# Performance work log

Measured on AMD Instinct MI355X. Metric: run time of the kernel, lower is better.

## Reference

```python
import jax, jax.numpy as jnp
import numpy as np

B, T, D = 4, 2048, 1024
H = 16
HD = D // H


def setup_inputs() -> dict:
    key = jax.random.key(0)
    ks = jax.random.split(key, 9)
    s = 1.0 / np.sqrt(D)
    return {
        "x": jax.random.normal(ks[0], (B, T, D), dtype=jnp.float32),
        "Wk": jax.random.normal(ks[1], (D, D), dtype=jnp.float32) * s,
        "bk": jnp.zeros((D,), dtype=jnp.float32),
        "Wq": jax.random.normal(ks[2], (D, D), dtype=jnp.float32) * s,
        "bq": jnp.zeros((D,), dtype=jnp.float32),
        "Wv": jax.random.normal(ks[3], (D, D), dtype=jnp.float32) * s,
        "bv": jnp.zeros((D,), dtype=jnp.float32),
        "Wp": jax.random.normal(ks[4], (D, D), dtype=jnp.float32) * s,
        "bp": jnp.zeros((D,), dtype=jnp.float32),
    }


def reference(x, Wk, bk, Wq, bq, Wv, bv, Wp, bp):
    Bv, Tv, Dv = x.shape
    # project and split heads: [B, H, T, HD]
    def heads(w, b):
        return (x @ w + b).reshape(Bv, Tv, H, HD).transpose(0, 2, 1, 3)
    k = heads(Wk, bk)
    q = heads(Wq, bq)
    v = heads(Wv, bv)
    scale = 1.0 / np.sqrt(HD)
    att = jnp.einsum('bhqd,bhkd->bhqk', q, k) * scale  # [B,H,T,T]
    causal = jnp.tril(jnp.ones((Tv, Tv), dtype=bool))
    att = jnp.where(causal[None, None, :, :], att, -jnp.inf)
    att = jax.nn.softmax(att, axis=-1)
    y = jnp.einsum('bhqk,bhkd->bhqd', att, v)  # [B,H,T,HD]
    y = y.transpose(0, 2, 1, 3).reshape(Bv, Tv, Dv)
    return y @ Wp + bp
```

## Files before the change

kernel.cpp:

```cpp
#include <hip/hip_runtime.h>
#include <stdint.h>

#define Bb 4
#define Tt 2048
#define Dd 1024
#define Hh 16
#define HDd 64
#define Mm 8192

typedef __attribute__((ext_vector_type(8))) short bf16x8;
typedef __attribute__((ext_vector_type(4))) float f32x4;
typedef __attribute__((ext_vector_type(16))) float f32x16;

#define MFMA(a, b, c) __builtin_amdgcn_mfma_f32_16x16x32_bf16(a, b, c, 0, 0, 0)
#define MFMA32(a, b, c) __builtin_amdgcn_mfma_f32_32x32x16_bf16(a, b, c, 0, 0, 0)

#define LOG2E 1.44269504088896340736f
#if __has_builtin(__builtin_amdgcn_exp2f)
#define EXP2(x) __builtin_amdgcn_exp2f(x)
#else
#define EXP2(x) __expf((x) * 0.69314718055994530942f)
#endif

union vfu { uint2 u2[2]; bf16x8 v; };
union apu { uint32_t u[4]; bf16x8 v; };

__device__ __forceinline__ unsigned short f2b(float f) {
  union { float f; uint32_t u; } v; v.f = f;
  return (unsigned short)((v.u + 0x7FFFu + ((v.u >> 16) & 1u)) >> 16);
}

__device__ __forceinline__ uint32_t pk2(float a, float b) {
  union { __bf16 h[2]; uint32_t u; } x;
  x.h[0] = (__bf16)a; x.h[1] = (__bf16)b;
  return x.u;
}

__device__ __forceinline__ void gload_lds16(const void* g, void* l) {
  __builtin_amdgcn_global_load_lds(
      (const __attribute__((address_space(1))) void*)g,
      (__attribute__((address_space(3))) void*)l, 16, 0, 0);
}

__global__ __launch_bounds__(256) void k_convert_x(const float* __restrict__ x,
                                                   unsigned short* __restrict__ xb) {
  int i = (blockIdx.x * 256 + threadIdx.x) * 8;
  float4 a = *(const float4*)(x + i);
  float4 b = *(const float4*)(x + i + 4);
  uint4 o;
  o.x = f2b(a.x) | ((uint32_t)f2b(a.y) << 16);
  o.y = f2b(a.z) | ((uint32_t)f2b(a.w) << 16);
  o.z = f2b(b.x) | ((uint32_t)f2b(b.y) << 16);
  o.w = f2b(b.z) | ((uint32_t)f2b(b.w) << 16);
  *(uint4*)(xb + i) = o;
}

__global__ __launch_bounds__(256) void k_transpose_w(
    const float* __restrict__ Wk, const float* __restrict__ Wq,
    const float* __restrict__ Wv, const float* __restrict__ Wp,
    unsigned short* __restrict__ WkT, unsigned short* __restrict__ WqT,
    unsigned short* __restrict__ WvT, unsigned short* __restrict__ WpT) {
  const float* W; unsigned short* O;
  int wsel = blockIdx.y;
  W = wsel == 0 ? Wk : wsel == 1 ? Wq : wsel == 2 ? Wv : Wp;
  O = wsel == 0 ? WkT : wsel == 1 ? WqT : wsel == 2 ? WvT : WpT;
  __shared__ unsigned short tile[32][36];
  int kb = (blockIdx.x >> 5) << 5;
  int nb = (blockIdx.x & 31) << 5;
  int t = threadIdx.x;
  int r = t >> 3, c4 = (t & 7) << 2;
  float4 v = *(const float4*)(W + (size_t)(kb + r) * Dd + nb + c4);
  tile[r][c4 + 0] = f2b(v.x); tile[r][c4 + 1] = f2b(v.y);
  tile[r][c4 + 2] = f2b(v.z); tile[r][c4 + 3] = f2b(v.w);
  __syncthreads();
  uint2 o;
  o.x = tile[c4 + 0][r] | ((uint32_t)tile[c4 + 1][r] << 16);
  o.y = tile[c4 + 2][r] | ((uint32_t)tile[c4 + 3][r] << 16);
  *(uint2*)(O + (size_t)(nb + r) * Dd + kb + c4) = o;
}

__global__ __launch_bounds__(256, 2) void k_gemm3(
    const unsigned short* __restrict__ A,
    const unsigned short* __restrict__ BtQ, const unsigned short* __restrict__ BtK,
    const unsigned short* __restrict__ BtV,
    const float* __restrict__ bq, const float* __restrict__ bk,
    const float* __restrict__ bv,
    unsigned short* __restrict__ Qb, unsigned short* __restrict__ Kb,
    unsigned short* __restrict__ VTb) {
  __shared__ __align__(16) unsigned short Al[128 * 32];
  __shared__ __align__(16) unsigned short Bl[3][128 * 32];
  int tid = threadIdx.x;
  int lane = tid & 63, wid = tid >> 6;
  int wr = wid >> 1, wc = wid & 1;
  int lq = lane & 15, lh = lane >> 4;
  int mb = blockIdx.x * 128;
  int nb = blockIdx.y << 7;

  int srow = (wid << 5) + (lane >> 2);
  int scol = (lane & 3) << 3;
  const unsigned short* Ag = A + (size_t)(mb + srow) * Dd + scol;
  const unsigned short* Bg0 = BtQ + (size_t)(nb + srow) * Dd + scol;
  const unsigned short* Bg1 = BtK + (size_t)(nb + srow) * Dd + scol;
  const unsigned short* Bg2 = BtV + (size_t)(nb + srow) * Dd + scol;
  unsigned short* Alw = Al + (wid << 10);
  unsigned short* Blw0 = &Bl[0][0] + (wid << 10);
  unsigned short* Blw1 = &Bl[1][0] + (wid << 10);
  unsigned short* Blw2 = &Bl[2][0] + (wid << 10);

  f32x4 zero = {0.f, 0.f, 0.f, 0.f};
  f32x4 acc[3][4][4];
#pragma unroll
  for (int s = 0; s < 3; s++)
#pragma unroll
    for (int m = 0; m < 4; m++)
#pragma unroll
      for (int n = 0; n < 4; n++) acc[s][m][n] = zero;

  for (int kb = 0; kb < Dd; kb += 32) {
    __syncthreads();
    gload_lds16(Ag + kb, Alw);
    gload_lds16(Ag + kb + 16 * Dd, Alw + 16 * 32);
    gload_lds16(Bg0 + kb, Blw0);
    gload_lds16(Bg0 + kb + 16 * Dd, Blw0 + 16 * 32);
    gload_lds16(Bg1 + kb, Blw1);
    gload_lds16(Bg1 + kb + 16 * Dd, Blw1 + 16 * 32);
    gload_lds16(Bg2 + kb, Blw2);
    gload_lds16(Bg2 + kb + 16 * Dd, Blw2 + 16 * 32);
    __syncthreads();
    bf16x8 af[4];
#pragma unroll
    for (int m = 0; m < 4; m++)
      af[m] = *(const bf16x8*)(Al + (((wr << 6) + (m << 4) + lq) << 5) + (lh << 3));
#pragma unroll
    for (int s = 0; s < 3; s++) {
      bf16x8 bf[4];
#pragma unroll
      for (int n = 0; n < 4; n++)
        bf[n] = *(const bf16x8*)(&Bl[s][0] +
                                 (((wc << 6) + (n << 4) + lq) << 5) + (lh << 3));
      __builtin_amdgcn_s_setprio(1);
#pragma unroll
      for (int m = 0; m < 4; m++)
#pragma unroll
        for (int n = 0; n < 4; n++) acc[s][m][n] = MFMA(af[m], bf[n], acc[s][m][n]);
      __builtin_amdgcn_s_setprio(0);
    }
  }

  int b_idx = mb >> 11;
#pragma unroll
  for (int s = 0; s < 3; s++) {
#pragma unroll
    for (int n = 0; n < 4; n++) {
      int col = nb + (wc << 6) + (n << 4) + lq;
      float bbias = (s == 0) ? bq[col] : (s == 1) ? bk[col] : bv[col];
      int hh = col >> 6, hd = col & 63;
#pragma unroll
      for (int m = 0; m < 4; m++) {
        int row0 = mb + (wr << 6) + (m << 4) + (lh << 2);
        int t0 = row0 & 2047;
        if (s == 2) {
          float v0 = acc[s][m][n][0] + bbias, v1 = acc[s][m][n][1] + bbias;
          float v2 = acc[s][m][n][2] + bbias, v3 = acc[s][m][n][3] + bbias;
          uint2 pv;
          pv.x = f2b(v0) | ((uint32_t)f2b(v1) << 16);
          pv.y = f2b(v2) | ((uint32_t)f2b(v3) << 16);
          int t0s = t0 ^ ((hd & 7) << 3);
          *(uint2*)(VTb + ((size_t)(b_idx * 16 + hh) * 64 + hd) * Tt + t0s) = pv;
        } else {
          unsigned short* O = (s == 0) ? Qb : Kb;
          float sc = (s == 0) ? (0.125f * LOG2E) : 1.0f;
#pragma unroll
          for (int r = 0; r < 4; r++) {
            float v = (acc[s][m][n][r] + bbias) * sc;
            int trow = t0 + r;
            int hds = (s == 0) ? hd : (hd ^ ((trow & 7) << 3));
            O[((size_t)(b_idx * 16 + hh) * Tt + trow) * 64 + hds] = f2b(v);
          }
        }
      }
    }
  }
}

__global__ __launch_bounds__(256) void k_gemm(
    const unsigned short* __restrict__ A,
    const unsigned short* __restrict__ Bt0,
    const float* __restrict__ bias0,
    float* __restrict__ Pout) {
  __shared__ __align__(16) unsigned short Al[128 * 32];
  __shared__ __align__(16) unsigned short Bl[128 * 32];
  int tid = threadIdx.x;
  int lane = tid & 63, wid = tid >> 6;
  int wr = wid >> 1, wc = wid & 1;
  int lq = lane & 15, lh = lane >> 4;
  int mb = blockIdx.x * 128;
  int nb = blockIdx.y << 7;
  const unsigned short* Bt = Bt0; const float* bias = bias0;

  int srow = (wid << 5) + (lane >> 2);
  int scol = (lane & 3) << 3;
  const unsigned short* Ag = A + (size_t)(mb + srow) * Dd + scol;
  const unsigned short* Bg = Bt + (size_t)(nb + srow) * Dd + scol;
  unsigned short* Alw = Al + (wid << 10);
  unsigned short* Blw = Bl + (wid << 10);

  f32x4 zero = {0.f, 0.f, 0.f, 0.f};
  f32x4 acc[4][4];
#pragma unroll
  for (int m = 0; m < 4; m++)
#pragma unroll
    for (int n = 0; n < 4; n++) acc[m][n] = zero;

  for (int kb = 0; kb < Dd; kb += 32) {
    __syncthreads();
    gload_lds16(Ag + kb, Alw);
    gload_lds16(Ag + kb + 16 * Dd, Alw + 16 * 32);
    gload_lds16(Bg + kb, Blw);
    gload_lds16(Bg + kb + 16 * Dd, Blw + 16 * 32);
    __syncthreads();
    bf16x8 af[4], bf[4];
#pragma unroll
    for (int m = 0; m < 4; m++)
      af[m] = *(const bf16x8*)(Al + (((wr << 6) + (m << 4) + lq) << 5) + (lh << 3));
#pragma unroll
    for (int n = 0; n < 4; n++)
      bf[n] = *(const bf16x8*)(Bl + (((wc << 6) + (n << 4) + lq) << 5) + (lh << 3));
#pragma unroll
    for (int m = 0; m < 4; m++)
#pragma unroll
      for (int n = 0; n < 4; n++) acc[m][n] = MFMA(af[m], bf[n], acc[m][n]);
  }

#pragma unroll
  for (int n = 0; n < 4; n++) {
    int col = nb + (wc << 6) + (n << 4) + lq;
    float bb = bias[col];
#pragma unroll
    for (int m = 0; m < 4; m++) {
      int row0 = mb + (wr << 6) + (m << 4) + (lh << 2);
#pragma unroll
      for (int r = 0; r < 4; r++)
        Pout[(size_t)(row0 + r) * Dd + col] = acc[m][n][r] + bb;
    }
  }
}

__global__ __launch_bounds__(256, 2) void k_attn(
    const unsigned short* __restrict__ Qb, const unsigned short* __restrict__ Kb,
    const unsigned short* __restrict__ VTb, unsigned short* __restrict__ yb) {
  __shared__ __align__(16) unsigned short KL[2][8192];
  __shared__ __align__(16) unsigned short VL[2][8192];
  int b = blockIdx.x;
  int qt = (b < 256) ? (7 - (b >> 6)) : ((b - 256) >> 6);
  int rr6 = b & 63;
  int bh = ((rr6 & 7) << 3) | (rr6 >> 3);
  int tid = threadIdx.x, lane = tid & 63, w = tid >> 6;
  int l31 = lane & 31, hi = lane >> 5;
  const unsigned short* __restrict__ Qh = Qb + (size_t)bh * Tt * 64;
  const unsigned short* __restrict__ Kh = Kb + (size_t)bh * Tt * 64;
  const unsigned short* __restrict__ Vh = VTb + (size_t)bh * 64 * Tt;
  int qgA = (qt << 8) + (w << 6);
  int qgB = qgA + 32;

  bf16x8 qfA[4], qfB[4];
#pragma unroll
  for (int c = 0; c < 4; c++) {
    qfA[c] = *(const bf16x8*)(Qh + (size_t)(qgA + l31) * 64 + (c << 4) + (hi << 3));
    qfB[c] = *(const bf16x8*)(Qh + (size_t)(qgB + l31) * 64 + (c << 4) + (hi << 3));
  }

  f32x16 accA0, accA1, accB0, accB1;
#pragma unroll
  for (int i = 0; i < 16; i++) { accA0[i] = 0.f; accA1[i] = 0.f; accB0[i] = 0.f; accB1[i] = 0.f; }
  float lsumA = 0.f, lsumB = 0.f;

  int jmaxb = (qt << 1) + 1;
  int srowK = lane >> 3, scolK = (lane & 7) << 3;
  int rowbK = w << 5;
  int srowV = lane >> 4, scolV = (lane & 15) << 3;
  int rowbV = w << 4;
  int swz = l31 & 7;

#define STAGE(kvt_, bi_) do {                                                        \
    int kv_ = (kvt_) << 7;                                                           \
    gload_lds16(Kh + (size_t)(kv_ + rowbK + srowK) * 64 + scolK,                     \
                &KL[bi_][rowbK << 6]);                                               \
    gload_lds16(Kh + (size_t)(kv_ + rowbK + 8 + srowK) * 64 + scolK,                 \
                &KL[bi_][(rowbK + 8) << 6]);                                         \
    gload_lds16(Kh + (size_t)(kv_ + rowbK + 16 + srowK) * 64 + scolK,                \
                &KL[bi_][(rowbK + 16) << 6]);                                        \
    gload_lds16(Kh + (size_t)(kv_ + rowbK + 24 + srowK) * 64 + scolK,                \
                &KL[bi_][(rowbK + 24) << 6]);                                        \
    gload_lds16(Vh + (size_t)(rowbV + srowV) * Tt + kv_ + scolV,                     \
                &VL[bi_][rowbV << 7]);                                               \
    gload_lds16(Vh + (size_t)(rowbV + 4 + srowV) * Tt + kv_ + scolV,                 \
                &VL[bi_][(rowbV + 4) << 7]);                                         \
    gload_lds16(Vh + (size_t)(rowbV + 8 + srowV) * Tt + kv_ + scolV,                 \
                &VL[bi_][(rowbV + 8) << 7]);                                         \
    gload_lds16(Vh + (size_t)(rowbV + 12 + srowV) * Tt + kv_ + scolV,                \
                &VL[bi_][(rowbV + 12) << 7]);                                        \
  } while (0)

  STAGE(0, 0);
  __syncthreads();

  int cur = 0;
  for (int jt = 0; jt <= jmaxb; ++jt) {
    if (jt < jmaxb) STAGE(jt + 1, cur ^ 1);
    int base_kv = jt << 7;
    if (qgB >= base_kv) {
      const unsigned short* KB = &KL[cur][0];
      const unsigned short* VB = &VL[cur][0];
#pragma unroll
      for (int n2 = 0; n2 < 4; n2++) {
        int rel_base = qgA - base_kv - (n2 << 5);
        if (rel_base >= -32) {
          bf16x8 kf[4];
          int krowb = ((n2 << 5) + l31) << 6;
#pragma unroll
          for (int c = 0; c < 4; c++)
            kf[c] = *(const bf16x8*)(KB + krowb + ((((c << 1) + hi) ^ swz) << 3));
          f32x16 sA, sB;
#pragma unroll
          for (int i = 0; i < 16; i++) { sA[i] = 0.f; sB[i] = 0.f; }
          __builtin_amdgcn_s_setprio(1);
#pragma unroll
          for (int c = 0; c < 4; c++) {
            sA = MFMA32(kf[c], qfA[c], sA);
            sB = MFMA32(kf[c], qfB[c], sB);
          }
          __builtin_amdgcn_s_setprio(0);
          float pA[16], pB[16];
          if (rel_base <= 0) {
            int relA = rel_base + l31, relB = relA + 32;
#pragma unroll
            for (int r = 0; r < 16; r++) {
              int krow = (r & 3) + ((r >> 2) << 3) + (hi << 2);
              pA[r] = EXP2(krow > relA ? -1e30f : sA[r]);
              pB[r] = EXP2(krow > relB ? -1e30f : sB[r]);
            }
          } else {
#pragma unroll
            for (int r = 0; r < 16; r++) { pA[r] = EXP2(sA[r]); pB[r] = EXP2(sB[r]); }
          }
          lsumA += (((pA[0] + pA[1]) + (pA[2] + pA[3])) + ((pA[4] + pA[5]) + (pA[6] + pA[7])))
                 + (((pA[8] + pA[9]) + (pA[10] + pA[11])) + ((pA[12] + pA[13]) + (pA[14] + pA[15])));
          lsumB += (((pB[0] + pB[1]) + (pB[2] + pB[3])) + ((pB[4] + pB[5]) + (pB[6] + pB[7])))
                 + (((pB[8] + pB[9]) + (pB[10] + pB[11])) + ((pB[12] + pB[13]) + (pB[14] + pB[15])));
          vfu vf[2][2];
#pragma unroll
          for (int n2v = 0; n2v < 2; n2v++) {
            int vrowb = ((n2v << 5) + l31) << 7;
#pragma unroll
            for (int cc = 0; cc < 2; cc++) {
              int blk0 = (n2 << 2) + (cc << 1);
              vf[n2v][cc].u2[0] =
                  *(const uint2*)(VB + vrowb + ((blk0 ^ swz) << 3) + (hi << 2));
              vf[n2v][cc].u2[1] =
                  *(const uint2*)(VB + vrowb + (((blk0 + 1) ^ swz) << 3) + (hi << 2));
            }
          }
          apu a0, a1, b0, b1;
#pragma unroll
          for (int g = 0; g < 4; g++) {
            a0.u[g] = pk2(pA[2 * g], pA[2 * g + 1]);
            a1.u[g] = pk2(pA[8 + 2 * g], pA[8 + 2 * g + 1]);
            b0.u[g] = pk2(pB[2 * g], pB[2 * g + 1]);
            b1.u[g] = pk2(pB[8 + 2 * g], pB[8 + 2 * g + 1]);
          }
          __builtin_amdgcn_s_setprio(1);
          accA0 = MFMA32(a0.v, vf[0][0].v, accA0);
          accA1 = MFMA32(a0.v, vf[1][0].v, accA1);
          accB0 = MFMA32(b0.v, vf[0][0].v, accB0);
          accB1 = MFMA32(b0.v, vf[1][0].v, accB1);
          accA0 = MFMA32(a1.v, vf[0][1].v, accA0);
          accA1 = MFMA32(a1.v, vf[1][1].v, accA1);
          accB0 = MFMA32(b1.v, vf[0][1].v, accB0);
          accB1 = MFMA32(b1.v, vf[1][1].v, accB1);
          __builtin_amdgcn_s_setprio(0);
        }
      }
    }
    __syncthreads();
    cur ^= 1;
  }
#undef STAGE

  lsumA += __shfl_xor(lsumA, 32);
  lsumB += __shfl_xor(lsumB, 32);
  float invA = 1.0f / lsumA;
  float invB = 1.0f / lsumB;
  int bb = bh >> 4, hh = bh & 15;
#pragma unroll
  for (int r = 0; r < 16; r++) {
    int qr = (r & 3) + ((r >> 2) << 3) + (hi << 2);
    float invqA = __shfl(invA, qr);
    float invqB = __shfl(invB, qr);
    size_t baseA = ((size_t)(bb * Tt + qgA + qr)) * Dd + (hh << 6) + l31;
    size_t baseB = ((size_t)(bb * Tt + qgB + qr)) * Dd + (hh << 6) + l31;
    yb[baseA] = f2b(accA0[r] * invqA);
    yb[baseA + 32] = f2b(accA1[r] * invqA);
    yb[baseB] = f2b(accB0[r] * invqB);
    yb[baseB + 32] = f2b(accB1[r] * invqB);
  }
}

extern "C" void kernel_launch(void* const* d_in, const int* in_sizes, int n_in,
                              void* d_out, int out_size, void* d_ws, size_t ws_size,
                              hipStream_t stream) {
  const float* x = (const float*)d_in[0];
  const float* Wk = (const float*)d_in[1];
  const float* bk = (const float*)d_in[2];
  const float* Wq = (const float*)d_in[3];
  const float* bq = (const float*)d_in[4];
  const float* Wv = (const float*)d_in[5];
  const float* bv = (const float*)d_in[6];
  const float* Wp = (const float*)d_in[7];
  const float* bp = (const float*)d_in[8];
  float* out = (float*)d_out;

  char* ws = (char*)d_ws;
  unsigned short* xb  = (unsigned short*)(ws);
  unsigned short* WkT = (unsigned short*)(ws + (16ull << 20));
  unsigned short* WqT = (unsigned short*)(ws + (18ull << 20));
  unsigned short* WvT = (unsigned short*)(ws + (20ull << 20));
  unsigned short* WpT = (unsigned short*)(ws + (22ull << 20));
  unsigned short* Qb  = (unsigned short*)(ws + (24ull << 20));
  unsigned short* Kb  = (unsigned short*)(ws + (40ull << 20));
  unsigned short* VTb = (unsigned short*)(ws + (56ull << 20));
  unsigned short* yb  = (unsigned short*)(ws + (72ull << 20));

  k_convert_x<<<4096, 256, 0, stream>>>(x, xb);
  k_transpose_w<<<dim3(1024, 4), 256, 0, stream>>>(Wk, Wq, Wv, Wp, WkT, WqT, WvT, WpT);
  k_gemm3<<<dim3(64, 8), 256, 0, stream>>>(xb, WqT, WkT, WvT, bq, bk, bv,
                                           Qb, Kb, VTb);
  k_attn<<<512, 256, 0, stream>>>(Qb, Kb, VTb, yb);
  k_gemm<<<dim3(64, 8), 256, 0, stream>>>(yb, WpT, bp, out);
}
```

Baseline: 159.8 us.

## Widen output GEMM tile, compute softmax sums via MFMA, skip masked-out tiles

The output projection GEMM now gives each block 256 columns held as two B tiles that share one A tile, with half as many blocks in y, so A-tile reuse doubles. The attention kernel computes the softmax row sums with an extra MFMA against a ones vector instead of scalar adds and shuffles. It also skips the A-half QK and PV MFMAs when that sub-tile lies entirely above the causal diagonal. This cuts VALU reductions and wasted MFMA work, at the cost of extra MFMAs and accumulator registers, and the GEMM now has fewer blocks.

After: 171.8 us. 1.08x slower.

```diff
diff --git a/kernel.cpp b/kernel.cpp
--- a/kernel.cpp
+++ b/kernel.cpp
@@ -183,65 +183,80 @@
   }
 }
 
-__global__ __launch_bounds__(256) void k_gemm(
+__global__ __launch_bounds__(256, 2) void k_gemm(
     const unsigned short* __restrict__ A,
     const unsigned short* __restrict__ Bt0,
     const float* __restrict__ bias0,
     float* __restrict__ Pout) {
   __shared__ __align__(16) unsigned short Al[128 * 32];
-  __shared__ __align__(16) unsigned short Bl[128 * 32];
+  __shared__ __align__(16) unsigned short Bl[2][128 * 32];
   int tid = threadIdx.x;
   int lane = tid & 63, wid = tid >> 6;
   int wr = wid >> 1, wc = wid & 1;
   int lq = lane & 15, lh = lane >> 4;
   int mb = blockIdx.x * 128;
-  int nb = blockIdx.y << 7;
-  const unsigned short* Bt = Bt0; const float* bias = bias0;
+  int nb = blockIdx.y << 8;
 
   int srow = (wid << 5) + (lane >> 2);
   int scol = (lane & 3) << 3;
   const unsigned short* Ag = A + (size_t)(mb + srow) * Dd + scol;
-  const unsigned short* Bg = Bt + (size_t)(nb + srow) * Dd + scol;
+  const unsigned short* Bg0 = Bt0 + (size_t)(nb + srow) * Dd + scol;
+  const unsigned short* Bg1 = Bt0 + (size_t)(nb + 128 + srow) * Dd + scol;
   unsigned short* Alw = Al + (wid << 10);
-  unsigned short* Blw = Bl + (wid << 10);
+  unsigned short* Blw0 = &Bl[0][0] + (wid << 10);
+  unsigned short* Blw1 = &Bl[1][0] + (wid << 10);
 
   f32x4 zero = {0.f, 0.f, 0.f, 0.f};
-  f32x4 acc[4][4];
-#pragma unroll
-  for (int m = 0; m < 4; m++)
-#pragma unroll
-    for (int n = 0; n < 4; n++) acc[m][n] = zero;
+  f32x4 acc[2][4][4];
+#pragma unroll
+  for (int p = 0; p < 2; p++)
+#pragma unroll
+    for (int m = 0; m < 4; m++)
+#pragma unroll
+      for (int n = 0; n < 4; n++) acc[p][m][n] = zero;
 
   for (int kb = 0; kb < Dd; kb += 32) {
     __syncthreads();
     gload_lds16(Ag + kb, Alw);
     gload_lds16(Ag + kb + 16 * Dd, Alw + 16 * 32);
-    gload_lds16(Bg + kb, Blw);
-    gload_lds16(Bg + kb + 16 * Dd, Blw + 16 * 32);
+    gload_lds16(Bg0 + kb, Blw0);
+    gload_lds16(Bg0 + kb + 16 * Dd, Blw0 + 16 * 32);
+    gload_lds16(Bg1 + kb, Blw1);
+    gload_lds16(Bg1 + kb + 16 * Dd, Blw1 + 16 * 32);
     __syncthreads();
-    bf16x8 af[4], bf[4];
+    bf16x8 af[4];
 #pragma unroll
     for (int m = 0; m < 4; m++)
       af[m] = *(const bf16x8*)(Al + (((wr << 6) + (m << 4) + lq) << 5) + (lh << 3));
 #pragma unroll
-    for (int n = 0; n < 4; n++)
-      bf[n] = *(const bf16x8*)(Bl + (((wc << 6) + (n << 4) + lq) << 5) + (lh << 3));
-#pragma unroll
-    for (int m = 0; m < 4; m++)
-#pragma unroll
-      for (int n = 0; n < 4; n++) acc[m][n] = MFMA(af[m], bf[n], acc[m][n]);
-  }
-
-#pragma unroll
-  for (int n = 0; n < 4; n++) {
-    int col = nb + (wc << 6) + (n << 4) + lq;
-    float bb = bias[col];
-#pragma unroll
-    for (int m = 0; m < 4; m++) {
-      int row0 = mb + (wr << 6) + (m << 4) + (lh << 2);
-#pragma unroll
-      for (int r = 0; r < 4; r++)
-        Pout[(size_t)(row0 + r) * Dd + col] = acc[m][n][r] + bb;
+    for (int p = 0; p < 2; p++) {
+      bf16x8 bf[4];
+#pragma unroll
+      for (int n = 0; n < 4; n++)
+        bf[n] = *(const bf16x8*)(&Bl[p][0] +
+                                 (((wc << 6) + (n << 4) + lq) << 5) + (lh << 3));
+      __builtin_amdgcn_s_setprio(1);
+#pragma unroll
+      for (int m = 0; m < 4; m++)
+#pragma unroll
+        for (int n = 0; n < 4; n++) acc[p][m][n] = MFMA(af[m], bf[n], acc[p][m][n]);
+      __builtin_amdgcn_s_setprio(0);
+    }
+  }
+
+#pragma unroll
+  for (int p = 0; p < 2; p++) {
+#pragma unroll
+    for (int n = 0; n < 4; n++) {
+      int col = nb + (p << 7) + (wc << 6) + (n << 4) + lq;
+      float bb = bias0[col];
+#pragma unroll
+      for (int m = 0; m < 4; m++) {
+        int row0 = mb + (wr << 6) + (m << 4) + (lh << 2);
+#pragma unroll
+        for (int r = 0; r < 4; r++)
+          Pout[(size_t)(row0 + r) * Dd + col] = acc[p][m][n][r] + bb;
+      }
     }
   }
 }
@@ -270,10 +285,14 @@
     qfB[c] = *(const bf16x8*)(Qh + (size_t)(qgB + l31) * 64 + (c << 4) + (hi << 3));
   }
 
-  f32x16 accA0, accA1, accB0, accB1;
-#pragma unroll
-  for (int i = 0; i < 16; i++) { accA0[i] = 0.f; accA1[i] = 0.f; accB0[i] = 0.f; accB1[i] = 0.f; }
-  float lsumA = 0.f, lsumB = 0.f;
+  f32x16 accA0, accA1, accB0, accB1, accLA, accLB;
+#pragma unroll
+  for (int i = 0; i < 16; i++) {
+    accA0[i] = 0.f; accA1[i] = 0.f; accB0[i] = 0.f; accB1[i] = 0.f;
+    accLA[i] = 0.f; accLB[i] = 0.f;
+  }
+  apu onesf;
+  onesf.u[0] = onesf.u[1] = onesf.u[2] = onesf.u[3] = 0x3F803F80u;
 
   int jmaxb = (qt << 1) + 1;
   int srowK = lane >> 3, scolK = (lane & 7) << 3;
@@ -316,6 +335,7 @@
       for (int n2 = 0; n2 < 4; n2++) {
         int rel_base = qgA - base_kv - (n2 << 5);
         if (rel_base >= -32) {
+          bool doA = (rel_base >= 0);
           bf16x8 kf[4];
           int krowb = ((n2 << 5) + l31) << 6;
 #pragma unroll
@@ -325,10 +345,15 @@
 #pragma unroll
           for (int i = 0; i < 16; i++) { sA[i] = 0.f; sB[i] = 0.f; }
           __builtin_amdgcn_s_setprio(1);
-#pragma unroll
-          for (int c = 0; c < 4; c++) {
-            sA = MFMA32(kf[c], qfA[c], sA);
-            sB = MFMA32(kf[c], qfB[c], sB);
+          if (doA) {
+#pragma unroll
+            for (int c = 0; c < 4; c++) {
+              sA = MFMA32(kf[c], qfA[c], sA);
+              sB = MFMA32(kf[c], qfB[c], sB);
+            }
+          } else {
+#pragma unroll
+            for (int c = 0; c < 4; c++) sB = MFMA32(kf[c], qfB[c], sB);
           }
           __builtin_amdgcn_s_setprio(0);
           float pA[16], pB[16];
@@ -337,17 +362,13 @@
 #pragma unroll
             for (int r = 0; r < 16; r++) {
               int krow = (r & 3) + ((r >> 2) << 3) + (hi << 2);
-              pA[r] = EXP2(krow > relA ? -1e30f : sA[r]);
+              if (doA) pA[r] = EXP2(krow > relA ? -1e30f : sA[r]);
               pB[r] = EXP2(krow > relB ? -1e30f : sB[r]);
             }
           } else {
 #pragma unroll
             for (int r = 0; r < 16; r++) { pA[r] = EXP2(sA[r]); pB[r] = EXP2(sB[r]); }
           }
-          lsumA += (((pA[0] + pA[1]) + (pA[2] + pA[3])) + ((pA[4] + pA[5]) + (pA[6] + pA[7])))
-                 + (((pA[8] + pA[9]) + (pA[10] + pA[11])) + ((pA[12] + pA[13]) + (pA[14] + pA[15])));
-          lsumB += (((pB[0] + pB[1]) + (pB[2] + pB[3])) + ((pB[4] + pB[5]) + (pB[6] + pB[7])))
-                 + (((pB[8] + pB[9]) + (pB[10] + pB[11])) + ((pB[12] + pB[13]) + (pB[14] + pB[15])));
           vfu vf[2][2];
 #pragma unroll
           for (int n2v = 0; n2v < 2; n2v++) {
@@ -361,24 +382,36 @@
                   *(const uint2*)(VB + vrowb + (((blk0 + 1) ^ swz) << 3) + (hi << 2));
             }
           }
-          apu a0, a1, b0, b1;
+          apu b0, b1;
 #pragma unroll
           for (int g = 0; g < 4; g++) {
-            a0.u[g] = pk2(pA[2 * g], pA[2 * g + 1]);
-            a1.u[g] = pk2(pA[8 + 2 * g], pA[8 + 2 * g + 1]);
             b0.u[g] = pk2(pB[2 * g], pB[2 * g + 1]);
             b1.u[g] = pk2(pB[8 + 2 * g], pB[8 + 2 * g + 1]);
           }
           __builtin_amdgcn_s_setprio(1);
-          accA0 = MFMA32(a0.v, vf[0][0].v, accA0);
-          accA1 = MFMA32(a0.v, vf[1][0].v, accA1);
           accB0 = MFMA32(b0.v, vf[0][0].v, accB0);
           accB1 = MFMA32(b0.v, vf[1][0].v, accB1);
-          accA0 = MFMA32(a1.v, vf[0][1].v, accA0);
-          accA1 = MFMA32(a1.v, vf[1][1].v, accA1);
+          accLB = MFMA32(b0.v, onesf.v, accLB);
           accB0 = MFMA32(b1.v, vf[0][1].v, accB0);
           accB1 = MFMA32(b1.v, vf[1][1].v, accB1);
+          accLB = MFMA32(b1.v, onesf.v, accLB);
           __builtin_amdgcn_s_setprio(0);
+          if (doA) {
+            apu a0, a1;
+#pragma unroll
+            for (int g = 0; g < 4; g++) {
+              a0.u[g] = pk2(pA[2 * g], pA[2 * g + 1]);
+              a1.u[g] = pk2(pA[8 + 2 * g], pA[8 + 2 * g + 1]);
+            }
+            __builtin_amdgcn_s_setprio(1);
+            accA0 = MFMA32(a0.v, vf[0][0].v, accA0);
+            accA1 = MFMA32(a0.v, vf[1][0].v, accA1);
+            accLA = MFMA32(a0.v, onesf.v, accLA);
+            accA0 = MFMA32(a1.v, vf[0][1].v, accA0);
+            accA1 = MFMA32(a1.v, vf[1][1].v, accA1);
+            accLA = MFMA32(a1.v, onesf.v, accLA);
+            __builtin_amdgcn_s_setprio(0);
+          }
         }
       }
     }
@@ -387,16 +420,12 @@
   }
 #undef STAGE
 
-  lsumA += __shfl_xor(lsumA, 32);
-  lsumB += __shfl_xor(lsumB, 32);
-  float invA = 1.0f / lsumA;
-  float invB = 1.0f / lsumB;
   int bb = bh >> 4, hh = bh & 15;
 #pragma unroll
   for (int r = 0; r < 16; r++) {
     int qr = (r & 3) + ((r >> 2) << 3) + (hi << 2);
-    float invqA = __shfl(invA, qr);
-    float invqB = __shfl(invB, qr);
+    float invqA = 1.0f / accLA[r];
+    float invqB = 1.0f / accLB[r];
     size_t baseA = ((size_t)(bb * Tt + qgA + qr)) * Dd + (hh << 6) + l31;
     size_t baseB = ((size_t)(bb * Tt + qgB + qr)) * Dd + (hh << 6) + l31;
     yb[baseA] = f2b(accA0[r] * invqA);
@@ -436,5 +465,5 @@
   k_gemm3<<<dim3(64, 8), 256, 0, stream>>>(xb, WqT, WkT, WvT, bq, bk, bv,
                                            Qb, Kb, VTb);
   k_attn<<<512, 256, 0, stream>>>(Qb, Kb, VTb, yb);
-  k_gemm<<<dim3(64, 8), 256, 0, stream>>>(yb, WpT, bp, out);
-}
+  k_gemm<<<dim3(64, 4), 256, 0, stream>>>(yb, WpT, bp, out);
+}
```
